# Kernel optimization log

Hardware: AMD Instinct MI355X
Metric: run time of the kernel (lower is better)

## Reference

```python
import math
import jax, jax.numpy as jnp
import numpy as np

B, S, D = 4, 2048, 1280
H, HD = 16, 80  # num_heads, head_dim
LOG2E = 1.442695041


def setup_inputs() -> dict:
    key = jax.random.key(0)
    ks = jax.random.split(key, 6)
    hidden_states = jax.random.normal(ks[0], (B, S, D), dtype=jnp.float32)
    # additive causal mask: 0 on/below diagonal, large negative above
    causal = jnp.tril(jnp.ones((S, S), dtype=bool))
    attention_mask = jnp.where(causal, 0.0, -1e9).astype(jnp.float32)[None, None, :, :]
    attention_mask = jnp.broadcast_to(attention_mask, (B, 1, S, S))
    scaling = jax.random.normal(ks[1], (HD,), dtype=jnp.float32)
    fan = 1.0 / math.sqrt(D)
    qkv_w = jax.random.normal(ks[2], (3 * H * HD, D), dtype=jnp.float32) * fan
    qkv_b = jax.random.normal(ks[3], (3 * H * HD,), dtype=jnp.float32) * fan
    o_w = jax.random.normal(ks[4], (D, H * HD), dtype=jnp.float32) * (1.0 / math.sqrt(H * HD))
    o_b = jax.random.normal(ks[5], (D,), dtype=jnp.float32) * fan
    return {
        "hidden_states": hidden_states,
        "attention_mask": attention_mask,
        "scaling": scaling,
        "qkv_w": qkv_w,
        "qkv_b": qkv_b,
        "o_w": o_w,
        "o_b": o_b,
    }


def reference(hidden_states, attention_mask, scaling, qkv_w, qkv_b, o_w, o_b):
    b, s, _ = hidden_states.shape
    qkv = hidden_states @ qkv_w.T + qkv_b  # [b, s, 3*H*HD]
    xq, xk, xv = jnp.split(qkv, [H * HD, 2 * H * HD], axis=-1)
    xq = xq.reshape(b, s, H, HD)
    xk = xk.reshape(b, s, H, HD)
    xv = xv.reshape(b, s, H, HD)
    # per-dim query scaling: softplus(scaling) * log2(e) / sqrt(head_dim)
    scale = jax.nn.softplus(scaling) * (LOG2E / math.sqrt(HD))
    xq = xq * scale[None, None, None, :]
    scores = jnp.einsum("bqhd,bkhd->bhqk", xq, xk) + attention_mask  # [b,H,s,s]
    probs = jax.nn.softmax(scores.astype(jnp.float32), axis=-1).astype(xq.dtype)
    out = jnp.einsum("bhqk,bkhd->bqhd", probs, xv).reshape(b, s, H * HD)
    return out @ o_w.T + o_b
```

## Files before the change

### kernel.cpp

```cpp
#include <hip/hip_runtime.h>
#include <math.h>

#define B_ 4
#define S_ 2048
#define D_ 1280
#define H_ 16
#define HD_ 80
#define HHD (H_ * HD_)
#define QKVN (3 * H_ * HD_)

typedef __bf16 bf16x8 __attribute__((ext_vector_type(8)));
typedef __bf16 bf16x4 __attribute__((ext_vector_type(4)));
typedef float  f32x4  __attribute__((ext_vector_type(4)));

__global__ __launch_bounds__(256) void cvt_bf16(
    const float* __restrict__ in, __bf16* __restrict__ out, int n8)
{
    const int i = blockIdx.x * 256 + threadIdx.x;
    if (i < n8) {
        const float4 a = ((const float4*)in)[2 * (size_t)i];
        const float4 b = ((const float4*)in)[2 * (size_t)i + 1];
        bf16x8 v = {(__bf16)a.x, (__bf16)a.y, (__bf16)a.z, (__bf16)a.w,
                    (__bf16)b.x, (__bf16)b.y, (__bf16)b.z, (__bf16)b.w};
        *(bf16x8*)(out + 8 * (size_t)i) = v;
    }
}

__device__ __forceinline__ void async_copy16(const void* g, void* l)
{
    __builtin_amdgcn_global_load_lds(
        (const __attribute__((address_space(1))) unsigned int*)g,
        (__attribute__((address_space(3))) unsigned int*)l, 16, 0, 0);
}

__device__ __forceinline__ void stage128x64(
    const __bf16* __restrict__ src, int K, char* lds, int tid)
{
    const int wave = tid >> 6, lane = tid & 63;
#pragma unroll
    for (int i = 0; i < 4; ++i) {
        const int c = (wave * 4 + i) * 64 + lane;
        const int r = c >> 3;
        const int g = (c & 7) ^ (r & 7);
        async_copy16(src + (size_t)r * K + g * 8, lds + (wave * 4 + i) * 1024);
    }
}

__device__ __forceinline__ bf16x8 frag_ld(const char* lds, int m, int j)
{
    return *(const bf16x8*)(lds + m * 128 + ((j ^ (m & 7)) << 4));
}

__device__ __forceinline__ void mfma_loop(
    const __bf16* __restrict__ A, const __bf16* __restrict__ W, int K,
    char* ldsA, char* ldsB, int tid, f32x4 acc[4][4])
{
    const int wave = tid >> 6;
    const int wm = wave >> 1, wn = wave & 1;
    const int l16 = tid & 15, quad = (tid & 63) >> 4;

#pragma unroll
    for (int mi = 0; mi < 4; ++mi)
#pragma unroll
        for (int ni = 0; ni < 4; ++ni) acc[mi][ni] = (f32x4){0.f, 0.f, 0.f, 0.f};

    for (int k0 = 0; k0 < K; k0 += 64) {
        __syncthreads();
        stage128x64(A + k0, K, ldsA, tid);
        stage128x64(W + k0, K, ldsB, tid);
        __syncthreads();
#pragma unroll
        for (int ks = 0; ks < 2; ++ks) {
            bf16x8 af[4], bfr[4];
#pragma unroll
            for (int mi = 0; mi < 4; ++mi)
                af[mi] = frag_ld(ldsA, wm * 64 + mi * 16 + l16, ks * 4 + quad);
#pragma unroll
            for (int ni = 0; ni < 4; ++ni)
                bfr[ni] = frag_ld(ldsB, wn * 64 + ni * 16 + l16, ks * 4 + quad);
#pragma unroll
            for (int mi = 0; mi < 4; ++mi)
#pragma unroll
                for (int ni = 0; ni < 4; ++ni)
                    acc[mi][ni] = __builtin_amdgcn_mfma_f32_16x16x32_bf16(
                        af[mi], bfr[ni], acc[mi][ni], 0, 0, 0);
        }
    }
}

__global__ __launch_bounds__(256) void gemm_qkv_mfma(
    const __bf16* __restrict__ Ab, const __bf16* __restrict__ Wb,
    const float* __restrict__ bias, const float* __restrict__ scaling,
    __bf16* __restrict__ Qb, __bf16* __restrict__ Kb, __bf16* __restrict__ Vtb)
{
    __shared__ __align__(16) char ldsA[128 * 128];
    __shared__ __align__(16) char ldsB[128 * 128];
    const int tid = threadIdx.x;
    const int m0 = blockIdx.y * 128, n0 = blockIdx.x * 128;

    f32x4 acc[4][4];
    mfma_loop(Ab + (size_t)m0 * D_, Wb + (size_t)n0 * D_, D_, ldsA, ldsB, tid, acc);

    const int wave = tid >> 6, wm = wave >> 1, wn = wave & 1;
    const int l16 = tid & 15, quad = (tid & 63) >> 4;
    const int sec = n0 / HHD;

#pragma unroll
    for (int ni = 0; ni < 4; ++ni) {
        const int col = n0 + wn * 64 + ni * 16 + l16;
        const int cis = col - sec * HHD;
        const int h = cis / HD_;
        const int d = cis - h * HD_;
        const float bv = bias[col];
        float qsv = 0.f;
        if (sec == 0)
            qsv = log1pf(expf(scaling[d])) *
                  (1.442695041f * 1.442695041f / 8.944271910f);
#pragma unroll
        for (int mi = 0; mi < 4; ++mi) {
#pragma unroll
            for (int r = 0; r < 4; ++r) {
                const int row = m0 + wm * 64 + mi * 16 + quad * 4 + r;
                const int bb = row >> 11;
                const int s = row & (S_ - 1);
                const size_t bh = (size_t)(bb * H_ + h);
                const float v = acc[mi][ni][r] + bv;
                if (sec == 0)      Qb[(bh * S_ + s) * HD_ + d] = (__bf16)(v * qsv);
                else if (sec == 1) Kb[(bh * S_ + s) * HD_ + d] = (__bf16)v;
                else               Vtb[(bh * HD_ + d) * S_ + s] = (__bf16)v;
            }
        }
    }
}

__global__ __launch_bounds__(256) void gemm_o_mfma(
    const __bf16* __restrict__ Ab, const __bf16* __restrict__ Wb,
    const float* __restrict__ bias, float* __restrict__ C)
{
    __shared__ __align__(16) char ldsA[128 * 128];
    __shared__ __align__(16) char ldsB[128 * 128];
    const int tid = threadIdx.x;
    const int m0 = blockIdx.y * 128, n0 = blockIdx.x * 128;

    f32x4 acc[4][4];
    mfma_loop(Ab + (size_t)m0 * D_, Wb + (size_t)n0 * D_, D_, ldsA, ldsB, tid, acc);

    const int wave = tid >> 6, wm = wave >> 1, wn = wave & 1;
    const int l16 = tid & 15, quad = (tid & 63) >> 4;

#pragma unroll
    for (int ni = 0; ni < 4; ++ni) {
        const int col = n0 + wn * 64 + ni * 16 + l16;
        const float bv = bias[col];
#pragma unroll
        for (int mi = 0; mi < 4; ++mi) {
#pragma unroll
            for (int r = 0; r < 4; ++r) {
                const int row = m0 + wm * 64 + mi * 16 + quad * 4 + r;
                C[(size_t)row * D_ + col] = acc[mi][ni][r] + bv;
            }
        }
    }
}

struct KF8 { bf16x8 f0, f1, f2; };

__device__ __forceinline__ void kload8(
    const __bf16* __restrict__ base, int row, int quad, KF8& kf)
{
    const __bf16* r = base + (size_t)row * HD_;
    kf.f0 = *(const bf16x8*)(r + quad * 8);
    kf.f1 = *(const bf16x8*)(r + 32 + quad * 8);
    bf16x8 z = {};
    if (quad < 2) z = *(const bf16x8*)(r + 64 + quad * 8);
    kf.f2 = z;
}

#define QK3(SREG, KF, QF)                                                      \
    SREG = __builtin_amdgcn_mfma_f32_16x16x32_bf16(KF.f0, QF.f0, SREG, 0, 0, 0); \
    SREG = __builtin_amdgcn_mfma_f32_16x16x32_bf16(KF.f1, QF.f1, SREG, 0, 0, 0); \
    SREG = __builtin_amdgcn_mfma_f32_16x16x32_bf16(KF.f2, QF.f2, SREG, 0, 0, 0);

#define MASK4(SREG, BASE, Q)                                                   \
    _Pragma("unroll")                                                          \
    for (int i = 0; i < 4; ++i)                                                \
        SREG[i] = ((BASE) + quad * 4 + i <= (Q) + l16) ? SREG[i] : -1e30f;

#define ATTN_BODY64(KT)                                                        \
    {                                                                          \
        const int k0 = (KT) * 64;                                              \
        const bool do_lo = ((KT) < nkt_lo);                  \
         \
        const bf16x8 vf00 = *(const bf16x8*)(Vbase + (size_t)( 0 + l16) * S_ + k0 + quad * 8);      \
        const bf16x8 vf01 = *(const bf16x8*)(Vbase + (size_t)( 0 + l16) * S_ + k0 + 32 + quad * 8); \
        const bf16x8 vf10 = *(const bf16x8*)(Vbase + (size_t)(16 + l16) * S_ + k0 + quad * 8);      \
        const bf16x8 vf11 = *(const bf16x8*)(Vbase + (size_t)(16 + l16) * S_ + k0 + 32 + quad * 8); \
        const bf16x8 vf20 = *(const bf16x8*)(Vbase + (size_t)(32 + l16) * S_ + k0 + quad * 8);      \
        const bf16x8 vf21 = *(const bf16x8*)(Vbase + (size_t)(32 + l16) * S_ + k0 + 32 + quad * 8); \
        const bf16x8 vf30 = *(const bf16x8*)(Vbase + (size_t)(48 + l16) * S_ + k0 + quad * 8);      \
        const bf16x8 vf31 = *(const bf16x8*)(Vbase + (size_t)(48 + l16) * S_ + k0 + 32 + quad * 8); \
        const bf16x8 vf40 = *(const bf16x8*)(Vbase + (size_t)(64 + l16) * S_ + k0 + quad * 8);      \
        const bf16x8 vf41 = *(const bf16x8*)(Vbase + (size_t)(64 + l16) * S_ + k0 + 32 + quad * 8); \
                          \
        f32x4 sH0 = (f32x4){0.f,0.f,0.f,0.f}, sH1 = sH0, sH2 = sH0, sH3 = sH0; \
        f32x4 sL0 = sH0, sL1 = sH0, sL2 = sH0, sL3 = sH0;                      \
        __builtin_amdgcn_s_setprio(1);                                         \
        QK3(sH0, kf0, qfH) QK3(sH1, kf1, qfH) QK3(sH2, kf2, qfH) QK3(sH3, kf3, qfH) \
        if (do_lo) {                                                           \
            QK3(sL0, kf0, qfL) QK3(sL1, kf1, qfL)                              \
            QK3(sL2, kf2, qfL) QK3(sL3, kf3, qfL)                              \
        }                                                                      \
        __builtin_amdgcn_s_setprio(0);                                         \
         \
         \
        {                                                                      \
            const int kn = ((KT) + 1 < nkt_hi ? (KT) + 1 : (KT)) * 64;         \
            kload8(Kbase, kn + l16, quad, kf0);                                \
            kload8(Kbase, kn + 16 + l16, quad, kf1);                           \
            kload8(Kbase, kn + 32 + l16, quad, kf2);                           \
            kload8(Kbase, kn + 48 + l16, quad, kf3);                           \
        }                                                                      \
                \
        float aH;                                                              \
        {                                                                      \
            if (k0 + 63 > q_hi) {                                              \
                MASK4(sH0, k0, q_hi)      MASK4(sH1, k0 + 16, q_hi)            \
                MASK4(sH2, k0 + 32, q_hi) MASK4(sH3, k0 + 48, q_hi)            \
            }                                                                  \
            float mA = fmaxf(fmaxf(sH0[0], sH0[1]), fmaxf(sH0[2], sH0[3]));    \
            float mB = fmaxf(fmaxf(sH1[0], sH1[1]), fmaxf(sH1[2], sH1[3]));    \
            float mC = fmaxf(fmaxf(sH2[0], sH2[1]), fmaxf(sH2[2], sH2[3]));    \
            float mD = fmaxf(fmaxf(sH3[0], sH3[1]), fmaxf(sH3[2], sH3[3]));    \
            float mx = fmaxf(fmaxf(mA, mB), fmaxf(mC, mD));                    \
            mx = fmaxf(mx, __shfl_xor(mx, 16));                                \
            mx = fmaxf(mx, __shfl_xor(mx, 32));                                \
            const float mn = fmaxf(mH, mx);                                    \
            aH = exp2f(mH - mn);                                               \
            mH = mn;                                                           \
            float rs = 0.f;                                                    \
            _Pragma("unroll")                                                  \
            for (int i = 0; i < 4; ++i) {                                      \
                const float p0 = exp2f(sH0[i] - mn);                           \
                const float p1 = exp2f(sH1[i] - mn);                           \
                const float p2 = exp2f(sH2[i] - mn);                           \
                const float p3 = exp2f(sH3[i] - mn);                           \
                sH0[i] = p0; sH1[i] = p1; sH2[i] = p2; sH3[i] = p3;            \
                rs += (p0 + p1) + (p2 + p3);                                   \
            }                                                                  \
            lH = lH * aH + rs;                           \
            *(bf16x4*)&Ps[wave][0][l16][0][quad * 4] =                         \
                (bf16x4){(__bf16)sH0[0], (__bf16)sH0[1], (__bf16)sH0[2], (__bf16)sH0[3]}; \
            *(bf16x4*)&Ps[wave][0][l16][0][16 + quad * 4] =                    \
                (bf16x4){(__bf16)sH1[0], (__bf16)sH1[1], (__bf16)sH1[2], (__bf16)sH1[3]}; \
            *(bf16x4*)&Ps[wave][0][l16][1][quad * 4] =                         \
                (bf16x4){(__bf16)sH2[0], (__bf16)sH2[1], (__bf16)sH2[2], (__bf16)sH2[3]}; \
            *(bf16x4*)&Ps[wave][0][l16][1][16 + quad * 4] =                    \
                (bf16x4){(__bf16)sH3[0], (__bf16)sH3[1], (__bf16)sH3[2], (__bf16)sH3[3]}; \
        }                                                                      \
                                          \
        float aL = 1.f;                                                        \
        if (do_lo) {                                                           \
            if (k0 + 63 > q_lo) {                                              \
                MASK4(sL0, k0, q_lo)      MASK4(sL1, k0 + 16, q_lo)            \
                MASK4(sL2, k0 + 32, q_lo) MASK4(sL3, k0 + 48, q_lo)            \
            }                                                                  \
            float mA = fmaxf(fmaxf(sL0[0], sL0[1]), fmaxf(sL0[2], sL0[3]));    \
            float mB = fmaxf(fmaxf(sL1[0], sL1[1]), fmaxf(sL1[2], sL1[3]));    \
            float mC = fmaxf(fmaxf(sL2[0], sL2[1]), fmaxf(sL2[2], sL2[3]));    \
            float mD = fmaxf(fmaxf(sL3[0], sL3[1]), fmaxf(sL3[2], sL3[3]));    \
            float mx = fmaxf(fmaxf(mA, mB), fmaxf(mC, mD));                    \
            mx = fmaxf(mx, __shfl_xor(mx, 16));                                \
            mx = fmaxf(mx, __shfl_xor(mx, 32));                                \
            const float mn = fmaxf(mL, mx);                                    \
            aL = exp2f(mL - mn);                                               \
            mL = mn;                                                           \
            float rs = 0.f;                                                    \
            _Pragma("unroll")                                                  \
            for (int i = 0; i < 4; ++i) {                                      \
                const float p0 = exp2f(sL0[i] - mn);                           \
                const float p1 = exp2f(sL1[i] - mn);                           \
                const float p2 = exp2f(sL2[i] - mn);                           \
                const float p3 = exp2f(sL3[i] - mn);                           \
                sL0[i] = p0; sL1[i] = p1; sL2[i] = p2; sL3[i] = p3;            \
                rs += (p0 + p1) + (p2 + p3);                                   \
            }                                                                  \
            lL = lL * aL + rs;                                                 \
            *(bf16x4*)&Ps[wave][1][l16][0][quad * 4] =                         \
                (bf16x4){(__bf16)sL0[0], (__bf16)sL0[1], (__bf16)sL0[2], (__bf16)sL0[3]}; \
            *(bf16x4*)&Ps[wave][1][l16][0][16 + quad * 4] =                    \
                (bf16x4){(__bf16)sL1[0], (__bf16)sL1[1], (__bf16)sL1[2], (__bf16)sL1[3]}; \
            *(bf16x4*)&Ps[wave][1][l16][1][quad * 4] =                         \
                (bf16x4){(__bf16)sL2[0], (__bf16)sL2[1], (__bf16)sL2[2], (__bf16)sL2[3]}; \
            *(bf16x4*)&Ps[wave][1][l16][1][16 + quad * 4] =                    \
                (bf16x4){(__bf16)sL3[0], (__bf16)sL3[1], (__bf16)sL3[2], (__bf16)sL3[3]}; \
        }                                                                      \
        asm volatile("s_waitcnt lgkmcnt(0)" ::: "memory");                     \
        const bf16x8 pfH0 = *(const bf16x8*)&Ps[wave][0][l16][0][quad * 8];    \
        const bf16x8 pfH1 = *(const bf16x8*)&Ps[wave][0][l16][1][quad * 8];    \
        const bf16x8 pfL0 = *(const bf16x8*)&Ps[wave][1][l16][0][quad * 8];    \
        const bf16x8 pfL1 = *(const bf16x8*)&Ps[wave][1][l16][1][quad * 8];    \
         \
        __builtin_amdgcn_s_setprio(1);                                         \
        {                                                                      \
            f32x4 c0, c1, c2, c3, c4;                                          \
            _Pragma("unroll")                                                  \
            for (int i = 0; i < 4; ++i) {                                      \
                c0[i] = oH0[i] * aH; c1[i] = oH1[i] * aH; c2[i] = oH2[i] * aH; \
                c3[i] = oH3[i] * aH; c4[i] = oH4[i] * aH;                      \
            }                                                                  \
            oH0 = __builtin_amdgcn_mfma_f32_16x16x32_bf16(vf00, pfH0, c0, 0, 0, 0); \
            oH1 = __builtin_amdgcn_mfma_f32_16x16x32_bf16(vf10, pfH0, c1, 0, 0, 0); \
            oH2 = __builtin_amdgcn_mfma_f32_16x16x32_bf16(vf20, pfH0, c2, 0, 0, 0); \
            oH3 = __builtin_amdgcn_mfma_f32_16x16x32_bf16(vf30, pfH0, c3, 0, 0, 0); \
            oH4 = __builtin_amdgcn_mfma_f32_16x16x32_bf16(vf40, pfH0, c4, 0, 0, 0); \
            oH0 = __builtin_amdgcn_mfma_f32_16x16x32_bf16(vf01, pfH1, oH0, 0, 0, 0); \
            oH1 = __builtin_amdgcn_mfma_f32_16x16x32_bf16(vf11, pfH1, oH1, 0, 0, 0); \
            oH2 = __builtin_amdgcn_mfma_f32_16x16x32_bf16(vf21, pfH1, oH2, 0, 0, 0); \
            oH3 = __builtin_amdgcn_mfma_f32_16x16x32_bf16(vf31, pfH1, oH3, 0, 0, 0); \
            oH4 = __builtin_amdgcn_mfma_f32_16x16x32_bf16(vf41, pfH1, oH4, 0, 0, 0); \
        }                                                                      \
        if (do_lo) {                                                           \
            f32x4 c0, c1, c2, c3, c4;                                          \
            _Pragma("unroll")                                                  \
            for (int i = 0; i < 4; ++i) {                                      \
                c0[i] = oL0[i] * aL; c1[i] = oL1[i] * aL; c2[i] = oL2[i] * aL; \
                c3[i] = oL3[i] * aL; c4[i] = oL4[i] * aL;                      \
            }                                                                  \
            oL0 = __builtin_amdgcn_mfma_f32_16x16x32_bf16(vf00, pfL0, c0, 0, 0, 0); \
            oL1 = __builtin_amdgcn_mfma_f32_16x16x32_bf16(vf10, pfL0, c1, 0, 0, 0); \
            oL2 = __builtin_amdgcn_mfma_f32_16x16x32_bf16(vf20, pfL0, c2, 0, 0, 0); \
            oL3 = __builtin_amdgcn_mfma_f32_16x16x32_bf16(vf30, pfL0, c3, 0, 0, 0); \
            oL4 = __builtin_amdgcn_mfma_f32_16x16x32_bf16(vf40, pfL0, c4, 0, 0, 0); \
            oL0 = __builtin_amdgcn_mfma_f32_16x16x32_bf16(vf01, pfL1, oL0, 0, 0, 0); \
            oL1 = __builtin_amdgcn_mfma_f32_16x16x32_bf16(vf11, pfL1, oL1, 0, 0, 0); \
            oL2 = __builtin_amdgcn_mfma_f32_16x16x32_bf16(vf21, pfL1, oL2, 0, 0, 0); \
            oL3 = __builtin_amdgcn_mfma_f32_16x16x32_bf16(vf31, pfL1, oL3, 0, 0, 0); \
            oL4 = __builtin_amdgcn_mfma_f32_16x16x32_bf16(vf41, pfL1, oL4, 0, 0, 0); \
        }                                                                      \
        __builtin_amdgcn_s_setprio(0);                                         \
    }

__global__ __launch_bounds__(256, 2) void attn_v13(
    const __bf16* __restrict__ Qb, const __bf16* __restrict__ Kb,
    const __bf16* __restrict__ Vtb, __bf16* __restrict__ out)
{
    __shared__ __align__(16) __bf16 Ps[4][2][16][2][40];

    const int tid = threadIdx.x;
    const int wave = tid >> 6;
    const int lane = tid & 63;
    const int l16 = lane & 15;
    const int quad = lane >> 4;

    const int flat = blockIdx.x;
    const int c = flat & 7;
    const int slot = flat >> 3;
    const int bhgrp = slot >> 4;
    const int xslot = slot & 15;
    const int bh = bhgrp * 8 + c;
    const int x = (xslot + 5 * bhgrp) & 15;
    const int b = bh >> 4, h = bh & 15;

    const int q_lo = 64 * x + 16 * wave;
    const int q_hi = 64 * (31 - x) + 16 * wave;

    const __bf16* Qbase = Qb + (size_t)bh * S_ * HD_;
    const __bf16* Kbase = Kb + (size_t)bh * S_ * HD_;
    const __bf16* Vbase = Vtb + (size_t)bh * HD_ * S_;

    KF8 qfL, qfH;
    kload8(Qbase, q_lo + l16, quad, qfL);
    kload8(Qbase, q_hi + l16, quad, qfH);

    float mL = -1e30f, lL = 0.f, mH = -1e30f, lH = 0.f;
    f32x4 oH0 = (f32x4){0.f,0.f,0.f,0.f}, oH1 = oH0, oH2 = oH0, oH3 = oH0, oH4 = oH0;
    f32x4 oL0 = oH0, oL1 = oH0, oL2 = oH0, oL3 = oH0, oL4 = oH0;

    const int nkt_lo = (q_lo + 16 + 63) >> 6;
    const int nkt_hi = (q_hi + 16 + 63) >> 6;

    KF8 kf0, kf1, kf2, kf3;
    kload8(Kbase, l16, quad, kf0);
    kload8(Kbase, 16 + l16, quad, kf1);
    kload8(Kbase, 32 + l16, quad, kf2);
    kload8(Kbase, 48 + l16, quad, kf3);

    for (int kt = 0; kt < nkt_hi; ++kt) {
        ATTN_BODY64(kt);
    }

    float lHs = lH + __shfl_xor(lH, 16);
    lHs += __shfl_xor(lHs, 32);
    float lLs = lL + __shfl_xor(lL, 16);
    lLs += __shfl_xor(lLs, 32);
    const float invH = 1.f / lHs;
    const float invL = 1.f / lLs;
    const size_t rowH = ((size_t)b * S_ + q_hi + l16) * HHD + h * HD_ + quad * 4;
    const size_t rowL = ((size_t)b * S_ + q_lo + l16) * HHD + h * HD_ + quad * 4;
    {
        bf16x4 v0 = {(__bf16)(oH0[0]*invH), (__bf16)(oH0[1]*invH), (__bf16)(oH0[2]*invH), (__bf16)(oH0[3]*invH)};
        bf16x4 v1 = {(__bf16)(oH1[0]*invH), (__bf16)(oH1[1]*invH), (__bf16)(oH1[2]*invH), (__bf16)(oH1[3]*invH)};
        bf16x4 v2 = {(__bf16)(oH2[0]*invH), (__bf16)(oH2[1]*invH), (__bf16)(oH2[2]*invH), (__bf16)(oH2[3]*invH)};
        bf16x4 v3 = {(__bf16)(oH3[0]*invH), (__bf16)(oH3[1]*invH), (__bf16)(oH3[2]*invH), (__bf16)(oH3[3]*invH)};
        bf16x4 v4 = {(__bf16)(oH4[0]*invH), (__bf16)(oH4[1]*invH), (__bf16)(oH4[2]*invH), (__bf16)(oH4[3]*invH)};
        *(bf16x4*)(out + rowH)      = v0;
        *(bf16x4*)(out + rowH + 16) = v1;
        *(bf16x4*)(out + rowH + 32) = v2;
        *(bf16x4*)(out + rowH + 48) = v3;
        *(bf16x4*)(out + rowH + 64) = v4;
    }
    {
        bf16x4 v0 = {(__bf16)(oL0[0]*invL), (__bf16)(oL0[1]*invL), (__bf16)(oL0[2]*invL), (__bf16)(oL0[3]*invL)};
        bf16x4 v1 = {(__bf16)(oL1[0]*invL), (__bf16)(oL1[1]*invL), (__bf16)(oL1[2]*invL), (__bf16)(oL1[3]*invL)};
        bf16x4 v2 = {(__bf16)(oL2[0]*invL), (__bf16)(oL2[1]*invL), (__bf16)(oL2[2]*invL), (__bf16)(oL2[3]*invL)};
        bf16x4 v3 = {(__bf16)(oL3[0]*invL), (__bf16)(oL3[1]*invL), (__bf16)(oL3[2]*invL), (__bf16)(oL3[3]*invL)};
        bf16x4 v4 = {(__bf16)(oL4[0]*invL), (__bf16)(oL4[1]*invL), (__bf16)(oL4[2]*invL), (__bf16)(oL4[3]*invL)};
        *(bf16x4*)(out + rowL)      = v0;
        *(bf16x4*)(out + rowL + 16) = v1;
        *(bf16x4*)(out + rowL + 32) = v2;
        *(bf16x4*)(out + rowL + 48) = v3;
        *(bf16x4*)(out + rowL + 64) = v4;
    }
}

extern "C" void kernel_launch(void* const* d_in, const int* in_sizes, int n_in,
                              void* d_out, int out_size, void* d_ws, size_t ws_size,
                              hipStream_t stream)
{
    const float* hidden  = (const float*)d_in[0];
    const float* scaling = (const float*)d_in[2];
    const float* qkv_w   = (const float*)d_in[3];
    const float* qkv_b   = (const float*)d_in[4];
    const float* o_w     = (const float*)d_in[5];
    const float* o_b     = (const float*)d_in[6];
    float* out = (float*)d_out;

    const size_t N_HID = (size_t)B_ * S_ * D_;
    const size_t N_QW  = (size_t)QKVN * D_;
    const size_t N_OW  = (size_t)D_ * D_;
    const size_t NPH   = (size_t)B_ * H_ * S_ * HD_;

    __bf16* Ab    = (__bf16*)d_ws;
    __bf16* Wqb   = Ab + N_HID;
    __bf16* Wob   = Wqb + N_QW;
    __bf16* Qb    = Wob + N_OW;
    __bf16* Kb    = Qb + NPH;
    __bf16* Vtb   = Kb + NPH;
    __bf16* attnb = Vtb + NPH;

    dim3 blk(256);

    cvt_bf16<<<dim3(N_HID / 8 / 256), blk, 0, stream>>>(hidden, Ab, N_HID / 8);
    cvt_bf16<<<dim3(N_QW  / 8 / 256), blk, 0, stream>>>(qkv_w, Wqb, N_QW / 8);
    cvt_bf16<<<dim3(N_OW  / 8 / 256), blk, 0, stream>>>(o_w,   Wob, N_OW / 8);

    gemm_qkv_mfma<<<dim3(QKVN / 128, B_ * S_ / 128), blk, 0, stream>>>(
        Ab, Wqb, qkv_b, scaling, Qb, Kb, Vtb);

    attn_v13<<<dim3(16 * H_ * B_), blk, 0, stream>>>(Qb, Kb, Vtb, attnb);

    gemm_o_mfma<<<dim3(D_ / 128, B_ * S_ / 128), blk, 0, stream>>>(
        attnb, Wob, o_b, out);
}
```

Measured before the change: 503.3 us.

## Remap GEMM blocks for XCD-local L2 reuse and vectorize V-transpose stores

Both GEMM kernels switch to a 1D grid whose block index is decoded so that each of the 8 XCDs handles a contiguous group of M-tiles, and tiles are grouped so blocks sharing A/B panels land on the same XCD's L2. The QKV epilogue for the V section now writes 4 consecutive sequence positions per thread as one bf16x4 store instead of 4 scalar strided stores. This is meant to cut L2 misses across chiplets and the uncoalesced transposed writes, at the cost of index arithmetic that depends on the grid being an exact multiple of the grouping.

Measured after the change: 476.6 us. 1.06x faster.

```diff
diff --git a/kernel.cpp b/kernel.cpp
--- a/kernel.cpp
+++ b/kernel.cpp
@@ -96,7 +96,16 @@
     __shared__ __align__(16) char ldsA[128 * 128];
     __shared__ __align__(16) char ldsB[128 * 128];
     const int tid = threadIdx.x;
-    const int m0 = blockIdx.y * 128, n0 = blockIdx.x * 128;
+
+    const int flat = blockIdx.x;
+    const int xcd = flat & 7;
+    const int idx = flat >> 3;
+    const int g = idx / 24;
+    const int r24 = idx - g * 24;
+    const int nn = r24 >> 3;
+    const int mm = r24 & 7;
+    const int m0 = (xcd * 8 + mm) * 128;
+    const int n0 = (g * 3 + nn) * 128;
 
     f32x4 acc[4][4];
     mfma_loop(Ab + (size_t)m0 * D_, Wb + (size_t)n0 * D_, D_, ldsA, ldsB, tid, acc);
@@ -105,29 +114,51 @@
     const int l16 = tid & 15, quad = (tid & 63) >> 4;
     const int sec = n0 / HHD;
 
-#pragma unroll
-    for (int ni = 0; ni < 4; ++ni) {
-        const int col = n0 + wn * 64 + ni * 16 + l16;
-        const int cis = col - sec * HHD;
-        const int h = cis / HD_;
-        const int d = cis - h * HD_;
-        const float bv = bias[col];
-        float qsv = 0.f;
-        if (sec == 0)
-            qsv = log1pf(expf(scaling[d])) *
-                  (1.442695041f * 1.442695041f / 8.944271910f);
-#pragma unroll
-        for (int mi = 0; mi < 4; ++mi) {
-#pragma unroll
-            for (int r = 0; r < 4; ++r) {
-                const int row = m0 + wm * 64 + mi * 16 + quad * 4 + r;
-                const int bb = row >> 11;
-                const int s = row & (S_ - 1);
+    if (sec == 2) {
+#pragma unroll
+        for (int ni = 0; ni < 4; ++ni) {
+            const int col = n0 + wn * 64 + ni * 16 + l16;
+            const int cis = col - 2 * HHD;
+            const int h = cis / HD_;
+            const int d = cis - h * HD_;
+            const float bv = bias[col];
+#pragma unroll
+            for (int mi = 0; mi < 4; ++mi) {
+                const int row0 = m0 + wm * 64 + mi * 16 + quad * 4;
+                const int bb = row0 >> 11;
+                const int s = row0 & (S_ - 1);
                 const size_t bh = (size_t)(bb * H_ + h);
-                const float v = acc[mi][ni][r] + bv;
-                if (sec == 0)      Qb[(bh * S_ + s) * HD_ + d] = (__bf16)(v * qsv);
-                else if (sec == 1) Kb[(bh * S_ + s) * HD_ + d] = (__bf16)v;
-                else               Vtb[(bh * HD_ + d) * S_ + s] = (__bf16)v;
+                bf16x4 pv = {(__bf16)(acc[mi][ni][0] + bv),
+                             (__bf16)(acc[mi][ni][1] + bv),
+                             (__bf16)(acc[mi][ni][2] + bv),
+                             (__bf16)(acc[mi][ni][3] + bv)};
+                *(bf16x4*)(Vtb + (bh * HD_ + d) * S_ + s) = pv;
+            }
+        }
+    } else {
+#pragma unroll
+        for (int ni = 0; ni < 4; ++ni) {
+            const int col = n0 + wn * 64 + ni * 16 + l16;
+            const int cis = col - sec * HHD;
+            const int h = cis / HD_;
+            const int d = cis - h * HD_;
+            const float bv = bias[col];
+            float qsv = 0.f;
+            if (sec == 0)
+                qsv = log1pf(expf(scaling[d])) *
+                      (1.442695041f * 1.442695041f / 8.944271910f);
+#pragma unroll
+            for (int mi = 0; mi < 4; ++mi) {
+#pragma unroll
+                for (int r = 0; r < 4; ++r) {
+                    const int row = m0 + wm * 64 + mi * 16 + quad * 4 + r;
+                    const int bb = row >> 11;
+                    const int s = row & (S_ - 1);
+                    const size_t bh = (size_t)(bb * H_ + h);
+                    const float v = acc[mi][ni][r] + bv;
+                    if (sec == 0) Qb[(bh * S_ + s) * HD_ + d] = (__bf16)(v * qsv);
+                    else          Kb[(bh * S_ + s) * HD_ + d] = (__bf16)v;
+                }
             }
         }
     }
@@ -140,7 +171,14 @@
     __shared__ __align__(16) char ldsA[128 * 128];
     __shared__ __align__(16) char ldsB[128 * 128];
     const int tid = threadIdx.x;
-    const int m0 = blockIdx.y * 128, n0 = blockIdx.x * 128;
+
+    const int flat = blockIdx.x;
+    const int xcd = flat & 7;
+    const int idx = flat >> 3;
+    const int mm = idx / 10;
+    const int nn = idx - mm * 10;
+    const int m0 = (xcd * 8 + mm) * 128;
+    const int n0 = nn * 128;
 
     f32x4 acc[4][4];
     mfma_loop(Ab + (size_t)m0 * D_, Wb + (size_t)n0 * D_, D_, ldsA, ldsB, tid, acc);
@@ -454,11 +492,11 @@
     cvt_bf16<<<dim3(N_QW  / 8 / 256), blk, 0, stream>>>(qkv_w, Wqb, N_QW / 8);
     cvt_bf16<<<dim3(N_OW  / 8 / 256), blk, 0, stream>>>(o_w,   Wob, N_OW / 8);
 
-    gemm_qkv_mfma<<<dim3(QKVN / 128, B_ * S_ / 128), blk, 0, stream>>>(
+    gemm_qkv_mfma<<<dim3(QKVN / 128 * (B_ * S_ / 128)), blk, 0, stream>>>(
         Ab, Wqb, qkv_b, scaling, Qb, Kb, Vtb);
 
     attn_v13<<<dim3(16 * H_ * B_), blk, 0, stream>>>(Qb, Kb, Vtb, attnb);
 
-    gemm_o_mfma<<<dim3(D_ / 128, B_ * S_ / 128), blk, 0, stream>>>(
+    gemm_o_mfma<<<dim3(D_ / 128 * (B_ * S_ / 128)), blk, 0, stream>>>(
         attnb, Wob, o_b, out);
 }
```
